# Kernel optimization log

Hardware: AMD Instinct MI355X
Metric: run time of the kernel (lower is better)

## Reference

```python
import jax, jax.numpy as jnp
import numpy as np

H = 128  # hidden_dim

def setup_inputs() -> dict:
    key = jax.random.key(0)
    ks = jax.random.split(key, 8)
    B, S = 32, 512
    return {
        "CNN_output": jax.random.normal(ks[0], (B, 4 * S, H), jnp.float32),
        "gaz_input": jax.random.normal(ks[1], (B, S, 128), jnp.float32),
        "gaz_input_back": jax.random.normal(ks[2], (B, S, 128), jnp.float32),
        "global_matrix": jax.random.normal(ks[3], (B, S, H), jnp.float32),
        "exper_input": jax.random.normal(ks[4], (B, S, H), jnp.float32),
        "W_cat": jax.random.normal(ks[5], (3 * H, 16 * H), jnp.float32) * (1.0 / np.sqrt(3 * H)),
        "b_cat": jnp.zeros((16 * H,), jnp.float32),
        "W_exp": jax.random.normal(ks[6], (H, 12 * H), jnp.float32) * (1.0 / np.sqrt(H)),
        "b_exp": jnp.zeros((12 * H,), jnp.float32),
    }


def _diag_gather(y, B, S, width):
    # y: [B, 4*S, 4*width]; for seq-block j pick columns j*width:(j+1)*width
    y = y.reshape(B, 4, S, 4, width)
    j = jnp.arange(4)
    y = y[:, j, :, j, :]              # [4, B, S, width]
    return jnp.transpose(y, (1, 0, 2, 3)).reshape(B, 4 * S, width)


def reference(CNN_output, gaz_input, gaz_input_back, global_matrix, exper_input,
              W_cat, b_cat, W_exp, b_exp):
    B, S4, _ = CNN_output.shape
    S = S4 // 4
    gaz = jnp.concatenate([gaz_input, gaz_input_back, gaz_input, gaz_input_back], axis=1)
    gm = jnp.tile(global_matrix, (1, 4, 1))
    exp_rep = jnp.tile(exper_input, (1, 4, 1))
    cat_in = jnp.concatenate([CNN_output, gaz, gm], axis=2)      # [B, 4S, 3H]
    cat_gates = _diag_gather(cat_in @ W_cat + b_cat, B, S, 4 * H)  # [B, 4S, 4H]
    exper_gates = _diag_gather(exp_rep @ W_exp + b_exp, B, S, 3 * H)  # [B, 4S, 3H]
    new_state = jnp.tanh(cat_gates[:, :, :H])
    gates = jax.nn.sigmoid(cat_gates[:, :, H:] + exper_gates)
    gates = jax.nn.softmax(gates.reshape(B, S4, 3, H), axis=2)
    state_cat = jnp.stack([new_state, CNN_output, exp_rep], axis=2)  # [B, 4S, 3, H]
    layer_output = jnp.sum(gates * state_cat, axis=2)                # [B, 4S, H]
    return tuple(layer_output[:, i * S:(i + 1) * S] for i in range(4))
```

## Files before the change

### kernel.cpp

```cpp
#include <hip/hip_runtime.h>

typedef unsigned short u16;
typedef unsigned int u32;
typedef short bf16x8 __attribute__((ext_vector_type(8)));
typedef float f32x4 __attribute__((ext_vector_type(4)));

#define HH 128

__device__ __forceinline__ u16 f2bf(float f) {
  u32 u = __float_as_uint(f);
  u += 0x7fffu + ((u >> 16) & 1u);
  return (u16)(u >> 16);
}
__device__ __forceinline__ u32 pack2(float a, float b) {
  return (u32)f2bf(a) | ((u32)f2bf(b) << 16);
}
__device__ __forceinline__ float bf2f(u16 h) {
  return __uint_as_float(((u32)h) << 16);
}

__global__ __launch_bounds__(256) void prep_w(const float* __restrict__ Wcat,
                                              const float* __restrict__ Wexp,
                                              u16* __restrict__ Wc) {
  const int bx = blockIdx.x;
  const int nt = bx & 7;
  const int kc = (bx >> 3) & 15;
  const int q = bx >> 7;
  __shared__ u16 T[32 * 72];

  const int tid = threadIdx.x;
  const int r = tid >> 3;
  const int c8 = (tid & 7) * 8;
  float v[8];
  if (kc < 12) {
    const float* src =
        Wcat + (size_t)(kc * 32 + r) * 2048 + q * 512 + nt * 64 + c8;
    float4 a = *(const float4*)src;
    float4 b = *(const float4*)(src + 4);
    v[0] = a.x; v[1] = a.y; v[2] = a.z; v[3] = a.w;
    v[4] = b.x; v[5] = b.y; v[6] = b.z; v[7] = b.w;
  } else if (nt >= 2) {
    const float* src = Wexp + (size_t)((kc - 12) * 32 + r) * 1536 + q * 384 +
                       nt * 64 + c8 - 128;
    float4 a = *(const float4*)src;
    float4 b = *(const float4*)(src + 4);
    v[0] = a.x; v[1] = a.y; v[2] = a.z; v[3] = a.w;
    v[4] = b.x; v[5] = b.y; v[6] = b.z; v[7] = b.w;
  } else {
#pragma unroll
    for (int j = 0; j < 8; ++j) v[j] = 0.f;
  }
  uint4 pk;
  pk.x = pack2(v[0], v[1]);
  pk.y = pack2(v[2], v[3]);
  pk.z = pack2(v[4], v[5]);
  pk.w = pack2(v[6], v[7]);
  *(uint4*)&T[r * 72 + c8] = pk;
  __syncthreads();

  const int p = tid & 3;
  const int nl = tid >> 2;
  const int lq = p ^ (nl & 3) ^ ((nl >> 2) & 3);
  u16 w[8];
#pragma unroll
  for (int j = 0; j < 8; ++j) w[j] = T[(lq * 8 + j) * 72 + nl];
  uint4 o;
  o.x = (u32)w[0] | ((u32)w[1] << 16);
  o.y = (u32)w[2] | ((u32)w[3] << 16);
  o.z = (u32)w[4] | ((u32)w[5] << 16);
  o.w = (u32)w[6] | ((u32)w[7] << 16);
  const size_t idx = ((size_t)((q * 16 + kc) * 512) + nt * 64 + nl) * 4 + p;
  ((uint4*)Wc)[idx] = o;
}

__global__ __launch_bounds__(512, 4) void fused_gate(
    const float* __restrict__ CNN, const float* __restrict__ gaz,
    const float* __restrict__ gazb, const float* __restrict__ gm,
    const float* __restrict__ exper, const u16* __restrict__ Wc,
    const float* __restrict__ bcat, const float* __restrict__ bexp,
    float* __restrict__ out) {
  __shared__ u16 Abuf[16 * 64 * 32];

  const int tid = threadIdx.x;
  const int lane = tid & 63;
  const int wave = tid >> 6;
  const int bx = blockIdx.x;
  const int tile = bx & 7;
  const int grp = bx >> 3;
  const int b = grp >> 2;
  const int q = grp & 3;
  const int s_base = tile * 64;

  const int arow = tid >> 3;
  const int ao = tid & 7;
  const int akcl = ao >> 2;
  const int aoo = ao & 3;
  const int asw = (arow & 3) ^ ((arow >> 2) & 3);
  const int cnnoff = (b * 2048 + q * 512 + s_base + arow) * HH;
  const int stdoff = (b * 512 + s_base + arow) * HH;
  const float* gz = (q & 1) ? gazb : gaz;

  {
    const float* sp = CNN + cnnoff + ao * 8;
    float4 f0 = *(const float4*)sp;
    float4 f1 = *(const float4*)(sp + 4);
    uint4 pk;
    pk.x = pack2(f0.x, f0.y);
    pk.y = pack2(f0.z, f0.w);
    pk.z = pack2(f1.x, f1.y);
    pk.w = pack2(f1.z, f1.w);
    const int kc = akcl;
    const int ph = aoo ^ asw;
    *(uint4*)&Abuf[(kc * 64 + arow) * 32 + ph * 8] = pk;
  }
  __syncthreads();

  const int l15 = lane & 15;
  const int quad = lane >> 4;
  const int sl = (l15 & 3) ^ ((l15 >> 2) & 3);
  const int physB = quad ^ sl;
  const u16* wq = Wc + q * 262144;
  int nofs[4];
#pragma unroll
  for (int gg = 0; gg < 4; ++gg)
    nofs[gg] = ((gg * 128 + wave * 16 + l15) * 4 + physB) * 8;

  f32x4 acc[4][4];
#pragma unroll
  for (int rt = 0; rt < 4; ++rt)
#pragma unroll
    for (int gg = 0; gg < 4; ++gg) acc[rt][gg] = (f32x4)0.f;

  bf16x8 bcur[4], bnxt[4];
#pragma unroll
  for (int gg = 0; gg < 4; ++gg) bcur[gg] = *(const bf16x8*)(wq + nofs[gg]);

#pragma unroll
  for (int c = 0; c < 8; ++c) {
    float4 f0, f1;
    if (c < 7) {
      const int cc = c + 1;
      const int sel = cc >> 1;
      const float* base = (sel == 0) ? CNN + cnnoff
                          : (sel == 1) ? gz + stdoff
                          : (sel == 2) ? gm + stdoff
                                       : exper + stdoff;
      const float* sp = base + (cc & 1) * 64 + ao * 8;
      f0 = *(const float4*)sp;
      f1 = *(const float4*)(sp + 4);
    }
#pragma unroll
    for (int k2 = 0; k2 < 2; ++k2) {
      const int kc = c * 2 + k2;
      if (kc < 15) {
#pragma unroll
        for (int gg = 0; gg < 4; ++gg)
          bnxt[gg] = *(const bf16x8*)(wq + (kc + 1) * 16384 + nofs[gg]);
      }
      const int pa = (quad ^ sl ^ (kc >> 2)) * 8;
      bf16x8 af[4];
#pragma unroll
      for (int rt = 0; rt < 4; ++rt)
        af[rt] = *(const bf16x8*)&Abuf[(kc * 64 + rt * 16 + l15) * 32 + pa];
#pragma unroll
      for (int rt = 0; rt < 4; ++rt)
#pragma unroll
        for (int gg = 0; gg < 4; ++gg)
          acc[rt][gg] = __builtin_amdgcn_mfma_f32_16x16x32_bf16(
              af[rt], bcur[gg], acc[rt][gg], 0, 0, 0);
#pragma unroll
      for (int gg = 0; gg < 4; ++gg) bcur[gg] = bnxt[gg];
    }
    if (c < 7) {
      uint4 pk;
      pk.x = pack2(f0.x, f0.y);
      pk.y = pack2(f0.z, f0.w);
      pk.z = pack2(f1.x, f1.y);
      pk.w = pack2(f1.z, f1.w);
      const int kc = (c + 1) * 2 + akcl;
      const int ph = aoo ^ asw ^ ((c + 1) >> 1);
      *(uint4*)&Abuf[(kc * 64 + arow) * 32 + ph * 8] = pk;
      __syncthreads();
    }
  }

  const float* bcq = bcat + q * 512;
  const float* beq = bexp + q * 384;
  const int outbase = ((q * 32 + b) * 512 + s_base) * HH;
  const int h = wave * 16 + l15;
  const float bc0 = bcq[h];
  const float bc1 = bcq[128 + h];
  const float bc2 = bcq[256 + h];
  const float bc3 = bcq[384 + h];
  const float be1 = beq[h];
  const float be2 = beq[128 + h];
  const float be3 = beq[256 + h];
  const int kcc = h >> 5;
  const int kce = 12 + (h >> 5);
  const int oh = (h >> 3) & 3;
  const int he = h & 7;
#pragma unroll
  for (int rt = 0; rt < 4; ++rt) {
#pragma unroll
    for (int r = 0; r < 4; ++r) {
      const int row = rt * 16 + quad * 4 + r;
      const int srw = (row & 3) ^ ((row >> 2) & 3);
      const float cnn = bf2f(Abuf[(kcc * 64 + row) * 32 + (oh ^ srw) * 8 + he]);
      const float ex =
          bf2f(Abuf[(kce * 64 + row) * 32 + (oh ^ srw ^ 3) * 8 + he]);
      const float c0 = acc[rt][0][r] + bc0;
      const float p1 = acc[rt][1][r] + bc1 + be1;
      const float p2 = acc[rt][2][r] + bc2 + be2;
      const float p3 = acc[rt][3][r] + bc3 + be3;
      const float e2c = __expf(2.f * c0);
      const float ns = 1.f - 2.f * __builtin_amdgcn_rcpf(e2c + 1.f);
      const float g1 = __builtin_amdgcn_rcpf(1.f + __expf(-p1));
      const float g2 = __builtin_amdgcn_rcpf(1.f + __expf(-p2));
      const float g3 = __builtin_amdgcn_rcpf(1.f + __expf(-p3));
      const float e1 = __expf(g1);
      const float e2 = __expf(g2);
      const float e3 = __expf(g3);
      const float inv = __builtin_amdgcn_rcpf(e1 + e2 + e3);
      out[outbase + row * HH + h] = (e1 * ns + e2 * cnn + e3 * ex) * inv;
    }
  }
}

extern "C" void kernel_launch(void* const* d_in, const int* in_sizes, int n_in,
                              void* d_out, int out_size, void* d_ws, size_t ws_size,
                              hipStream_t stream) {
  const float* CNN = (const float*)d_in[0];
  const float* gaz = (const float*)d_in[1];
  const float* gazb = (const float*)d_in[2];
  const float* gm = (const float*)d_in[3];
  const float* exper = (const float*)d_in[4];
  const float* Wcat = (const float*)d_in[5];
  const float* bcat = (const float*)d_in[6];
  const float* Wexp = (const float*)d_in[7];
  const float* bexp = (const float*)d_in[8];
  u16* Wc = (u16*)d_ws;

  prep_w<<<512, 256, 0, stream>>>(Wcat, Wexp, Wc);
  fused_gate<<<1024, 512, 0, stream>>>(CNN, gaz, gazb, gm, exper, Wc, bcat,
                                       bexp, (float*)d_out);
}
```

Baseline: 178.5 us.

## Restructure A-tile staging into two halves with a single mid-loop barrier

The A tile is now staged differently. Before the main loop each thread loads and stores the CNN and gaz halves (eight K-chunks) with narrower float4 loads. The gm and exper halves are then streamed in one float4 per iteration while the first eight K-chunks are computed. This swaps the seven per-iteration __syncthreads for a single barrier between the two halves. The MFMA issue is also split into pairs of row tiles to reduce live A-fragment registers. The costs are more global load instructions, each of 16 bytes, and a larger up-front load burst before the first MFMA.

Result: faster. 158.4 us (-11.3%).

```diff
diff --git a/kernel.cpp b/kernel.cpp
--- a/kernel.cpp
+++ b/kernel.cpp
@@ -92,26 +92,31 @@
   const int s_base = tile * 64;
 
   const int arow = tid >> 3;
-  const int ao = tid & 7;
-  const int akcl = ao >> 2;
-  const int aoo = ao & 3;
+  const int slot = tid & 7;
   const int asw = (arow & 3) ^ ((arow >> 2) & 3);
-  const int cnnoff = (b * 2048 + q * 512 + s_base + arow) * HH;
-  const int stdoff = (b * 512 + s_base + arow) * HH;
+  const int p0 = (slot >> 1) ^ asw;
+  const int half4 = (slot & 1) * 4;
+  const int cnnoff = (b * 2048 + q * 512 + s_base + arow) * HH + slot * 4;
+  const int stdoff = (b * 512 + s_base + arow) * HH + slot * 4;
   const float* gz = (q & 1) ? gazb : gaz;
 
+  float4 fcur = *(const float4*)(gm + stdoff);
+
   {
-    const float* sp = CNN + cnnoff + ao * 8;
-    float4 f0 = *(const float4*)sp;
-    float4 f1 = *(const float4*)(sp + 4);
-    uint4 pk;
-    pk.x = pack2(f0.x, f0.y);
-    pk.y = pack2(f0.z, f0.w);
-    pk.z = pack2(f1.x, f1.y);
-    pk.w = pack2(f1.z, f1.w);
-    const int kc = akcl;
-    const int ph = aoo ^ asw;
-    *(uint4*)&Abuf[(kc * 64 + arow) * 32 + ph * 8] = pk;
+    float4 f[8];
+#pragma unroll
+    for (int j = 0; j < 4; ++j)
+      f[j] = *(const float4*)(CNN + cnnoff + j * 32);
+#pragma unroll
+    for (int j = 4; j < 8; ++j)
+      f[j] = *(const float4*)(gz + stdoff + (j - 4) * 32);
+#pragma unroll
+    for (int j = 0; j < 8; ++j) {
+      uint2 v;
+      v.x = pack2(f[j].x, f[j].y);
+      v.y = pack2(f[j].z, f[j].w);
+      *(uint2*)&Abuf[(j * 64 + arow) * 32 + (p0 ^ (j >> 2)) * 8 + half4] = v;
+    }
   }
   __syncthreads();
 
@@ -136,52 +141,89 @@
   for (int gg = 0; gg < 4; ++gg) bcur[gg] = *(const bf16x8*)(wq + nofs[gg]);
 
 #pragma unroll
-  for (int c = 0; c < 8; ++c) {
-    float4 f0, f1;
-    if (c < 7) {
-      const int cc = c + 1;
-      const int sel = cc >> 1;
-      const float* base = (sel == 0) ? CNN + cnnoff
-                          : (sel == 1) ? gz + stdoff
-                          : (sel == 2) ? gm + stdoff
-                                       : exper + stdoff;
-      const float* sp = base + (cc & 1) * 64 + ao * 8;
-      f0 = *(const float4*)sp;
-      f1 = *(const float4*)(sp + 4);
-    }
-#pragma unroll
-    for (int k2 = 0; k2 < 2; ++k2) {
-      const int kc = c * 2 + k2;
-      if (kc < 15) {
-#pragma unroll
-        for (int gg = 0; gg < 4; ++gg)
-          bnxt[gg] = *(const bf16x8*)(wq + (kc + 1) * 16384 + nofs[gg]);
-      }
-      const int pa = (quad ^ sl ^ (kc >> 2)) * 8;
-      bf16x8 af[4];
-#pragma unroll
-      for (int rt = 0; rt < 4; ++rt)
-        af[rt] = *(const bf16x8*)&Abuf[(kc * 64 + rt * 16 + l15) * 32 + pa];
-#pragma unroll
-      for (int rt = 0; rt < 4; ++rt)
-#pragma unroll
-        for (int gg = 0; gg < 4; ++gg)
-          acc[rt][gg] = __builtin_amdgcn_mfma_f32_16x16x32_bf16(
-              af[rt], bcur[gg], acc[rt][gg], 0, 0, 0);
-#pragma unroll
-      for (int gg = 0; gg < 4; ++gg) bcur[gg] = bnxt[gg];
-    }
-    if (c < 7) {
-      uint4 pk;
-      pk.x = pack2(f0.x, f0.y);
-      pk.y = pack2(f0.z, f0.w);
-      pk.z = pack2(f1.x, f1.y);
-      pk.w = pack2(f1.z, f1.w);
-      const int kc = (c + 1) * 2 + akcl;
-      const int ph = aoo ^ asw ^ ((c + 1) >> 1);
-      *(uint4*)&Abuf[(kc * 64 + arow) * 32 + ph * 8] = pk;
-      __syncthreads();
-    }
+  for (int kc = 0; kc < 8; ++kc) {
+    float4 fnxt;
+    if (kc < 7) {
+      const int j = kc + 1;
+      const float* sp = (j < 4) ? gm : exper;
+      fnxt = *(const float4*)(sp + stdoff + (j & 3) * 32);
+    }
+#pragma unroll
+    for (int gg = 0; gg < 4; ++gg)
+      bnxt[gg] = *(const bf16x8*)(wq + (kc + 1) * 16384 + nofs[gg]);
+
+    const int pa = (quad ^ sl ^ (kc >> 2)) * 8;
+    {
+      bf16x8 a0 = *(const bf16x8*)&Abuf[(kc * 64 + l15) * 32 + pa];
+      bf16x8 a1 = *(const bf16x8*)&Abuf[(kc * 64 + 16 + l15) * 32 + pa];
+#pragma unroll
+      for (int gg = 0; gg < 4; ++gg)
+        acc[0][gg] = __builtin_amdgcn_mfma_f32_16x16x32_bf16(a0, bcur[gg],
+                                                             acc[0][gg], 0, 0, 0);
+#pragma unroll
+      for (int gg = 0; gg < 4; ++gg)
+        acc[1][gg] = __builtin_amdgcn_mfma_f32_16x16x32_bf16(a1, bcur[gg],
+                                                             acc[1][gg], 0, 0, 0);
+    }
+    {
+      bf16x8 a2 = *(const bf16x8*)&Abuf[(kc * 64 + 32 + l15) * 32 + pa];
+      bf16x8 a3 = *(const bf16x8*)&Abuf[(kc * 64 + 48 + l15) * 32 + pa];
+#pragma unroll
+      for (int gg = 0; gg < 4; ++gg)
+        acc[2][gg] = __builtin_amdgcn_mfma_f32_16x16x32_bf16(a2, bcur[gg],
+                                                             acc[2][gg], 0, 0, 0);
+#pragma unroll
+      for (int gg = 0; gg < 4; ++gg)
+        acc[3][gg] = __builtin_amdgcn_mfma_f32_16x16x32_bf16(a3, bcur[gg],
+                                                             acc[3][gg], 0, 0, 0);
+    }
+    {
+      const int dk = 8 + kc;
+      uint2 v;
+      v.x = pack2(fcur.x, fcur.y);
+      v.y = pack2(fcur.z, fcur.w);
+      *(uint2*)&Abuf[(dk * 64 + arow) * 32 + (p0 ^ (dk >> 2)) * 8 + half4] = v;
+      fcur = fnxt;
+    }
+#pragma unroll
+    for (int gg = 0; gg < 4; ++gg) bcur[gg] = bnxt[gg];
+  }
+  __syncthreads();
+
+#pragma unroll
+  for (int kc = 8; kc < 16; ++kc) {
+    if (kc < 15) {
+#pragma unroll
+      for (int gg = 0; gg < 4; ++gg)
+        bnxt[gg] = *(const bf16x8*)(wq + (kc + 1) * 16384 + nofs[gg]);
+    }
+    const int pa = (quad ^ sl ^ (kc >> 2)) * 8;
+    {
+      bf16x8 a0 = *(const bf16x8*)&Abuf[(kc * 64 + l15) * 32 + pa];
+      bf16x8 a1 = *(const bf16x8*)&Abuf[(kc * 64 + 16 + l15) * 32 + pa];
+#pragma unroll
+      for (int gg = 0; gg < 4; ++gg)
+        acc[0][gg] = __builtin_amdgcn_mfma_f32_16x16x32_bf16(a0, bcur[gg],
+                                                             acc[0][gg], 0, 0, 0);
+#pragma unroll
+      for (int gg = 0; gg < 4; ++gg)
+        acc[1][gg] = __builtin_amdgcn_mfma_f32_16x16x32_bf16(a1, bcur[gg],
+                                                             acc[1][gg], 0, 0, 0);
+    }
+    {
+      bf16x8 a2 = *(const bf16x8*)&Abuf[(kc * 64 + 32 + l15) * 32 + pa];
+      bf16x8 a3 = *(const bf16x8*)&Abuf[(kc * 64 + 48 + l15) * 32 + pa];
+#pragma unroll
+      for (int gg = 0; gg < 4; ++gg)
+        acc[2][gg] = __builtin_amdgcn_mfma_f32_16x16x32_bf16(a2, bcur[gg],
+                                                             acc[2][gg], 0, 0, 0);
+#pragma unroll
+      for (int gg = 0; gg < 4; ++gg)
+        acc[3][gg] = __builtin_amdgcn_mfma_f32_16x16x32_bf16(a3, bcur[gg],
+                                                             acc[3][gg], 0, 0, 0);
+    }
+#pragma unroll
+    for (int gg = 0; gg < 4; ++gg) bcur[gg] = bnxt[gg];
   }
 
   const float* bcq = bcat + q * 512;
@@ -204,7 +246,7 @@
 #pragma unroll
     for (int r = 0; r < 4; ++r) {
       const int row = rt * 16 + quad * 4 + r;
-      const int srw = (row & 3) ^ ((row >> 2) & 3);
+      const int srw = r ^ quad;
       const float cnn = bf2f(Abuf[(kcc * 64 + row) * 32 + (oh ^ srw) * 8 + he]);
       const float ex =
           bf2f(Abuf[(kce * 64 + row) * 32 + (oh ^ srw ^ 3) * 8 + he]);
```
